# Optimization experiments

Hardware: AMD Instinct MI355X
Metric: run time of the kernel (lower is better)

Reference implementation:

```python
import jax, jax.numpy as jnp
import numpy as np

B, T, I, H = 128, 2048, 32, 64  # batch, seq_len, input_size, hidden_size
FF_SCALE = 0.001


def setup_inputs() -> dict:
    key = jax.random.key(0)
    ks = jax.random.split(key, 8)
    f32 = jnp.float32
    return {
        "x": jax.random.normal(ks[0], (B, T, I), f32),
        # forward-direction RNN params (torch layout: W_ih [H,I], W_hh [H,H])
        "W_ih_f": jax.random.normal(ks[1], (H, I), f32) * FF_SCALE,
        "W_hh_f": jnp.eye(H, dtype=f32),  # eye_ init * hidden_scale=1.0
        "b_ih_f": jnp.zeros((H,), f32),
        "b_hh_f": jnp.zeros((H,), f32),
        # backward-direction RNN params
        "W_ih_b": jax.random.normal(ks[2], (H, I), f32) * FF_SCALE,
        "W_hh_b": jnp.eye(H, dtype=f32),
        "b_ih_b": jnp.zeros((H,), f32),
        "b_hh_b": jnp.zeros((H,), f32),
        # MLP head: Linear(2H,2H) + leaky_relu + Linear(2H,1)
        "ff0_w": jax.random.normal(ks[3], (2 * H, 2 * H), f32) * FF_SCALE,
        "ff0_b": jnp.zeros((2 * H,), f32),
        "ff1_w": jax.random.normal(ks[4], (1, 2 * H), f32) * FF_SCALE,
        "ff1_b": jnp.zeros((1,), f32),
    }


def _rnn_dir(x, W_ih, W_hh, b_ih, b_hh, reverse):
    # Precompute input projection for all timesteps: [B,T,H]
    xw = jnp.einsum('bti,hi->bth', x, W_ih) + b_ih + b_hh

    def step(h, xt):
        h = jax.nn.relu(xt + h @ W_hh.T)
        return h, h

    h0 = jnp.zeros((x.shape[0], W_hh.shape[0]), x.dtype)
    # scan over time ([T,B,H]); reverse=True = reversed input + reversed output,
    # exactly the backward direction of a bidirectional RNN.
    _, hs = jax.lax.scan(step, h0, jnp.swapaxes(xw, 0, 1), reverse=reverse)
    return jnp.swapaxes(hs, 0, 1)  # [B,T,H]


def reference(x, W_ih_f, W_hh_f, b_ih_f, b_hh_f,
              W_ih_b, W_hh_b, b_ih_b, b_hh_b,
              ff0_w, ff0_b, ff1_w, ff1_b):
    hf = _rnn_dir(x, W_ih_f, W_hh_f, b_ih_f, b_hh_f, reverse=False)
    hb = _rnn_dir(x, W_ih_b, W_hh_b, b_ih_b, b_hh_b, reverse=True)
    h = jnp.concatenate([hf, hb], axis=-1)  # [B,T,2H]
    out = jax.nn.leaky_relu(h @ ff0_w.T + ff0_b, negative_slope=0.01)
    out = out @ ff1_w.T + ff1_b  # [B,T,1]
    return out
```

## Files before the change

kernel.cpp:

```cpp
#include <hip/hip_runtime.h>

#define BB 128
#define TT 2048
#define II 32
#define HH 64

typedef __attribute__((ext_vector_type(8))) short bf16x8;
typedef __attribute__((ext_vector_type(4))) float f32x4;

__device__ __forceinline__ unsigned f2bf(float f) {
    unsigned u = __builtin_bit_cast(unsigned, f);
    return (u + 0x7fffu + ((u >> 16) & 1u)) >> 16;
}

__device__ __forceinline__ unsigned cvtpk(float lo, float hi) {
    unsigned r;
    asm("v_cvt_pk_bf16_f32 %0, %1, %2" : "=v"(r) : "v"(lo), "v"(hi));
    return r;
}

__device__ __forceinline__ int swzW(int r, int t) {
    return (((r << 10) + t) ^ (((t >> 5) & 31) << 2)) ^ ((r & 7) << 2);
}

#define FWD_SEQ(M) \
  M(q0.x) M(q0.y) M(q0.z) M(q0.w) M(q1.x) M(q1.y) M(q1.z) M(q1.w) \
  M(q2.x) M(q2.y) M(q2.z) M(q2.w) M(q3.x) M(q3.y) M(q3.z) M(q3.w) \
  M(q4.x) M(q4.y) M(q4.z) M(q4.w) M(q5.x) M(q5.y) M(q5.z) M(q5.w) \
  M(q6.x) M(q6.y) M(q6.z) M(q6.w) M(q7.x) M(q7.y) M(q7.z) M(q7.w)
#define BWD_SEQ(M) \
  M(q7.w) M(q7.z) M(q7.y) M(q7.x) M(q6.w) M(q6.z) M(q6.y) M(q6.x) \
  M(q5.w) M(q5.z) M(q5.y) M(q5.x) M(q4.w) M(q4.z) M(q4.y) M(q4.x) \
  M(q3.w) M(q3.z) M(q3.y) M(q3.x) M(q2.w) M(q2.z) M(q2.y) M(q2.x) \
  M(q1.w) M(q1.z) M(q1.y) M(q1.x) M(q0.w) M(q0.z) M(q0.y) M(q0.x)

template<int DIR>
__device__ __noinline__ void rnn_serial_f(
    const float* __restrict__ Wih, const float* __restrict__ bih,
    const float* __restrict__ bhh, const float* __restrict__ Whh,
    const float* __restrict__ x, unsigned short* __restrict__ hbuf,
    int b, int lane, float (*hs)[HH])
{
    const float bias = bih[lane] + bhh[lane];
    const float4* wip = (const float4*)(Wih + lane * II);
    const float4* whp = (const float4*)(Whh + lane * HH);
    hs[0][lane] = 0.0f;
    unsigned short* hb = hbuf + ((size_t)(DIR * BB + b) * HH + lane) * TT;
    int cur = 0;
    for (int s = 0; s < TT; ++s) {
        const int t = DIR ? (TT - 1 - s) : s;
        const float4* xr = (const float4*)(x + ((size_t)b * TT + t) * II);
        float a0 = bias, a1 = 0.f, a2 = 0.f, a3 = 0.f;
        #pragma unroll
        for (int i4 = 0; i4 < II / 4; ++i4) {
            const float4 w4 = wip[i4];
            const float4 v  = xr[i4];
            a0 = fmaf(w4.x, v.x, a0); a1 = fmaf(w4.y, v.y, a1);
            a2 = fmaf(w4.z, v.z, a2); a3 = fmaf(w4.w, v.w, a3);
        }
        float s0 = 0.f, s1 = 0.f, s2 = 0.f, s3 = 0.f;
        const float* hc = hs[cur];
        #pragma unroll
        for (int j4 = 0; j4 < HH / 4; ++j4) {
            const float4 w4 = whp[j4];
            const float4 h4 = *(const float4*)(hc + 4 * j4);
            s0 = fmaf(w4.x, h4.x, s0); s1 = fmaf(w4.y, h4.y, s1);
            s2 = fmaf(w4.z, h4.z, s2); s3 = fmaf(w4.w, h4.w, s3);
        }
        const float h = fmaxf((a0 + a1) + (a2 + a3) + ((s0 + s1) + (s2 + s3)), 0.0f);
        hs[cur ^ 1][lane] = h;
        hb[t] = (unsigned short)f2bf(h);
        cur ^= 1;
    }
}

__global__ __launch_bounds__(512, 4) void rnn_fused_kernel(
    const float* __restrict__ x,
    const float* __restrict__ Wf, const float* __restrict__ bihf, const float* __restrict__ bhhf,
    const float* __restrict__ Wb, const float* __restrict__ bihb, const float* __restrict__ bhhb,
    const float* __restrict__ Whf, const float* __restrict__ Whb,
    unsigned short* __restrict__ hbuf)
{
    __shared__ __align__(16) float xwsh[8 * 1024];
    __shared__ __align__(16) unsigned short xst[2][8][512];
    __shared__ float sflags[2];
    __shared__ __align__(16) float hshd[2][2][HH];

    const int tid  = threadIdx.x;
    const int lane = tid & 63;
    const int wv   = __builtin_amdgcn_readfirstlane(tid >> 6);
    const int blk  = blockIdx.x;
    const int xcd  = blk & 7;
    const int rank = blk >> 3;
    const int b    = ((rank >> 4) << 3) | xcd;
    const int g    = rank & 15;
    const int g4   = g << 2;

    if (wv < 2) {
        const float* W = wv ? Whb : Whf;
        bool ok = true;
        const float4* wp = (const float4*)(W + lane * HH);
        #pragma unroll
        for (int j4 = 0; j4 < HH / 4; ++j4) {
            float4 v = wp[j4];
            ok &= (v.x == ((4*j4+0 == lane) ? 1.0f : 0.0f));
            ok &= (v.y == ((4*j4+1 == lane) ? 1.0f : 0.0f));
            ok &= (v.z == ((4*j4+2 == lane) ? 1.0f : 0.0f));
            ok &= (v.w == ((4*j4+3 == lane) ? 1.0f : 0.0f));
        }
        const bool isI = (__ballot(ok) == ~0ull);
        if (lane == 0) sflags[wv] = isI ? 1.0f : 0.0f;
    }
    __syncthreads();
    const bool iF = sflags[0] != 0.0f;
    const bool iB = sflags[1] != 0.0f;

    if (iF | iB) {
        bf16x8 afrag;
        {
            const int m = lane & 15, kg = lane >> 4;
            uint4 ap = {0u, 0u, 0u, 0u};
            if (m < 8) {
                const float* Wrow = ((m < 4) ? (Wf + (g4 + m) * II)
                                             : (Wb + (g4 + m - 4) * II)) + kg * 8;
                const float4 wa = *(const float4*)Wrow;
                const float4 wc = *(const float4*)(Wrow + 4);
                ap.x = cvtpk(wa.x, wa.y);
                ap.y = cvtpk(wa.z, wa.w);
                ap.z = cvtpk(wc.x, wc.y);
                ap.w = cvtpk(wc.z, wc.w);
            }
            afrag = __builtin_bit_cast(bf16x8, ap);
        }
        f32x4 cbias;
        {
            const int r0 = lane >> 4;
            #pragma unroll
            for (int j = 0; j < 4; ++j) {
                const int m = r0 * 4 + j;
                float v = 0.0f;
                if (m < 4)      v = bihf[g4 + m] + bhhf[g4 + m];
                else if (m < 8) v = bihb[g4 + m - 4] + bhhb[g4 + m - 4];
                cbias[j] = v;
            }
        }

        #define STAGE(BUFI, V0, V1) {                                           \
            unsigned short* bp_ = xst[BUFI][wv];                                \
            const int base_ = ((lane >> 3) << 5) + ((lane & 7) << 2);           \
            uint2 p_;                                                           \
            p_.x = cvtpk(V0.x, V0.y);                                           \
            p_.y = cvtpk(V0.z, V0.w);                                           \
            *(uint2*)(bp_ + base_) = p_;                                        \
            p_.x = cvtpk(V1.x, V1.y);                                           \
            p_.y = cvtpk(V1.z, V1.w);                                           \
            *(uint2*)(bp_ + base_ + 256) = p_;                                  \
        }

        float4 q0 = {0,0,0,0}, q1 = {0,0,0,0}, q2 = {0,0,0,0}, q3 = {0,0,0,0},
               q4 = {0,0,0,0}, q5 = {0,0,0,0}, q6 = {0,0,0,0}, q7 = {0,0,0,0};

        const float4* xb4 = (const float4*)(x + (size_t)b * TT * II) + (wv << 7);
        {
            const float4 a0 = xb4[lane], a1 = xb4[lane + 64];
            STAGE(0, a0, a1)
        }
        float4 va0 = xb4[1024 + lane], va1 = xb4[1024 + lane + 64];
        float4 vb0 = xb4[2048 + lane], vb1 = xb4[2048 + lane + 64];

        #pragma unroll
        for (int cc = 0; cc < 16; ++cc) {
            if (cc == 8) {
                __syncthreads();
                if ((lane >> 5) == 0) {
                    const int tb = (lane & 31) << 5;
                    q0 = *(const float4*)(xwsh + swzW(wv, tb + 0));
                    q1 = *(const float4*)(xwsh + swzW(wv, tb + 4));
                    q2 = *(const float4*)(xwsh + swzW(wv, tb + 8));
                    q3 = *(const float4*)(xwsh + swzW(wv, tb + 12));
                    q4 = *(const float4*)(xwsh + swzW(wv, tb + 16));
                    q5 = *(const float4*)(xwsh + swzW(wv, tb + 20));
                    q6 = *(const float4*)(xwsh + swzW(wv, tb + 24));
                    q7 = *(const float4*)(xwsh + swzW(wv, tb + 28));
                }
                __syncthreads();
            }
            const bf16x8 bfrag = *(const bf16x8*)(xst[cc & 1][wv] +
                ((lane & 15) << 5) + ((lane >> 4) << 3));
            float4 na0, na1;
            if (cc < 13) {
                const float4* gp = xb4 + ((cc + 3) << 10);
                na0 = gp[lane]; na1 = gp[lane + 64];
            }
            if (cc < 15) { STAGE((cc + 1) & 1, va0, va1) }
            {
                f32x4 accv = __builtin_amdgcn_mfma_f32_16x16x32_bf16(afrag, bfrag, cbias, 0, 0, 0);
                if (lane < 32) {
                    const int th = ((cc & 7) << 7) + (wv << 4) + (lane & 15);
                    const int m0 = (lane >> 4) << 2;
                    xwsh[swzW(m0 + 0, th)] = accv[0];
                    xwsh[swzW(m0 + 1, th)] = accv[1];
                    xwsh[swzW(m0 + 2, th)] = accv[2];
                    xwsh[swzW(m0 + 3, th)] = accv[3];
                }
            }
            va0 = vb0; va1 = vb1;
            vb0 = na0; vb1 = na1;
        }
        #undef STAGE

        __syncthreads();
        if ((lane >> 5) == 1) {
            const int tb = (lane & 31) << 5;
            q0 = *(const float4*)(xwsh + swzW(wv, tb + 0));
            q1 = *(const float4*)(xwsh + swzW(wv, tb + 4));
            q2 = *(const float4*)(xwsh + swzW(wv, tb + 8));
            q3 = *(const float4*)(xwsh + swzW(wv, tb + 12));
            q4 = *(const float4*)(xwsh + swzW(wv, tb + 16));
            q5 = *(const float4*)(xwsh + swzW(wv, tb + 20));
            q6 = *(const float4*)(xwsh + swzW(wv, tb + 24));
            q7 = *(const float4*)(xwsh + swzW(wv, tb + 28));
        }

        const int dir  = wv >> 2;
        const int hrow = g4 + (wv & 3);
        const bool en  = dir ? iB : iF;
        if (en) {
            float A = 0.0f, Bv = -__builtin_inff();
            #define CSTEP(c) { A = A + (c); Bv = fmaxf(Bv + (c), 0.0f); }
            if (dir == 0) { FWD_SEQ(CSTEP) } else { BWD_SEQ(CSTEP) }
            #undef CSTEP

            float h;
            if (dir == 0) {
                #pragma unroll
                for (int off = 1; off < 64; off <<= 1) {
                    float Au = __shfl_up(A,  (unsigned)off);
                    float Bu = __shfl_up(Bv, (unsigned)off);
                    if (lane >= off) {
                        Bv = fmaxf(Bu + A, Bv);
                        A  = Au + A;
                    }
                }
                float Ae = __shfl_up(A, 1u);
                float Be = __shfl_up(Bv, 1u);
                h = (lane == 0) ? 0.0f : fmaxf(Ae, Be);
            } else {
                #pragma unroll
                for (int off = 1; off < 64; off <<= 1) {
                    float Au = __shfl_down(A,  (unsigned)off);
                    float Bu = __shfl_down(Bv, (unsigned)off);
                    if (lane < 64 - off) {
                        Bv = fmaxf(Bu + A, Bv);
                        A  = Au + A;
                    }
                }
                float Ae = __shfl_down(A, 1u);
                float Be = __shfl_down(Bv, 1u);
                h = (lane == 63) ? 0.0f : fmaxf(Ae, Be);
            }

            #define ASTEP(c) { h = fmaxf(h + (c), 0.0f); (c) = h; }
            if (dir == 0) { FWD_SEQ(ASTEP) } else { BWD_SEQ(ASTEP) }
            #undef ASTEP

            unsigned short* hb = hbuf + ((size_t)(dir * BB + b) * HH + hrow) * TT + (lane << 5);
            uint4 s0q, s1q, s2q, s3q;
            s0q.x = cvtpk(q0.x, q0.y); s0q.y = cvtpk(q0.z, q0.w);
            s0q.z = cvtpk(q1.x, q1.y); s0q.w = cvtpk(q1.z, q1.w);
            s1q.x = cvtpk(q2.x, q2.y); s1q.y = cvtpk(q2.z, q2.w);
            s1q.z = cvtpk(q3.x, q3.y); s1q.w = cvtpk(q3.z, q3.w);
            s2q.x = cvtpk(q4.x, q4.y); s2q.y = cvtpk(q4.z, q4.w);
            s2q.z = cvtpk(q5.x, q5.y); s2q.w = cvtpk(q5.z, q5.w);
            s3q.x = cvtpk(q6.x, q6.y); s3q.y = cvtpk(q6.z, q6.w);
            s3q.z = cvtpk(q7.x, q7.y); s3q.w = cvtpk(q7.z, q7.w);
            uint4* hv = (uint4*)hb;
            hv[0] = s0q; hv[1] = s1q; hv[2] = s2q; hv[3] = s3q;
        }
    }

    if (!iF && g == 0 && wv == 0)
        rnn_serial_f<0>(Wf, bihf, bhhf, Whf, x, hbuf, b, lane, hshd[0]);
    if (!iB && g == 0 && wv == 1)
        rnn_serial_f<1>(Wb, bihb, bhhb, Whb, x, hbuf, b, lane, hshd[1]);
}

__global__ __launch_bounds__(256) void mlp_kernel(
    const unsigned short* __restrict__ hbuf,
    const float* __restrict__ w0, const float* __restrict__ b0,
    const float* __restrict__ w1, const float* __restrict__ b1,
    float* __restrict__ out)
{
    const int tid  = threadIdx.x;
    const int lane = tid & 63;
    const int wv   = tid >> 6;
    const int blk  = blockIdx.x;
    const int b    = blk >> 5;
    const int t0   = (blk & 31) << 6;

    __shared__ __align__(16) unsigned int w0dw[128 * 64];
    __shared__ __align__(16) unsigned int hsh[128 * 32];

    #pragma unroll
    for (int it = 0; it < 16; ++it) {
        const int q = it * 256 + tid;
        const float4 v = ((const float4*)w0)[q];
        uint2 p;
        p.x = cvtpk(v.x, v.y);
        p.y = cvtpk(v.z, v.w);
        const int k  = q >> 5;
        const int dw = (k << 6) + ((q & 31) << 1);
        *(uint2*)(w0dw + (dw ^ ((k & 15) << 2))) = p;
    }

    #pragma unroll
    for (int it = 0; it < 4; ++it) {
        const int q   = it * 256 + tid;
        const int j   = q >> 3, sub = q & 7;
        const unsigned short* rp =
            hbuf + ((size_t)((j >> 6) * BB + b) * HH + (j & 63)) * TT + t0;
        const uint4 v = *(const uint4*)(rp + sub * 8);
        const int dwb = j * 32 + sub * 4;
        *(uint4*)(hsh + (dwb ^ (((j >> 3) & 3) << 3))) = v;
    }
    __syncthreads();

    const int lg = lane >> 4;
    const int tl = (wv << 4) + (lane & 15);
    const int t  = t0 + tl;
    const int m  = lane & 15;

    f32x4 acc[8];
    #pragma unroll
    for (int kt = 0; kt < 8; ++kt) {
        const float4 v = *(const float4*)(b0 + kt * 16 + lg * 4);
        acc[kt][0] = v.x; acc[kt][1] = v.y; acc[kt][2] = v.z; acc[kt][3] = v.w;
    }

    const unsigned short* hus = (const unsigned short*)hsh;
    #pragma unroll
    for (int jt = 0; jt < 4; ++jt) {
        bf16x8 bf;
        #pragma unroll
        for (int i = 0; i < 8; ++i) {
            const int j  = jt * 32 + lg * 8 + i;
            const int dw = (j * 32 + (tl >> 1)) ^ (lg << 3);
            bf[i] = (short)hus[dw * 2 + (tl & 1)];
        }
        #pragma unroll
        for (int kt = 0; kt < 8; ++kt) {
            const int krow = kt * 16 + m;
            const bf16x8 af = *(const bf16x8*)(w0dw +
                ((((krow << 6) + (jt << 4) + (lg << 2)) ^ ((krow & 15) << 2))));
            acc[kt] = __builtin_amdgcn_mfma_f32_16x16x32_bf16(af, bf, acc[kt], 0, 0, 0);
        }
    }

    float o = 0.0f;
    #pragma unroll
    for (int kt = 0; kt < 8; ++kt) {
        const float4 wq = *(const float4*)(w1 + kt * 16 + lg * 4);
        float v0 = acc[kt][0]; v0 = fmaxf(v0, 0.01f * v0); o = fmaf(v0, wq.x, o);
        float v1 = acc[kt][1]; v1 = fmaxf(v1, 0.01f * v1); o = fmaf(v1, wq.y, o);
        float v2 = acc[kt][2]; v2 = fmaxf(v2, 0.01f * v2); o = fmaf(v2, wq.z, o);
        float v3 = acc[kt][3]; v3 = fmaxf(v3, 0.01f * v3); o = fmaf(v3, wq.w, o);
    }
    o += __shfl_xor(o, 16);
    o += __shfl_xor(o, 32);
    if (lg == 0) out[(size_t)b * TT + t] = o + b1[0];
}

extern "C" void kernel_launch(void* const* d_in, const int* in_sizes, int n_in,
                              void* d_out, int out_size, void* d_ws, size_t ws_size,
                              hipStream_t stream) {
    (void)in_sizes; (void)n_in; (void)out_size; (void)ws_size;
    const float* x    = (const float*)d_in[0];
    const float* Wihf = (const float*)d_in[1];
    const float* Whhf = (const float*)d_in[2];
    const float* bihf = (const float*)d_in[3];
    const float* bhhf = (const float*)d_in[4];
    const float* Wihb = (const float*)d_in[5];
    const float* Whhb = (const float*)d_in[6];
    const float* bihb = (const float*)d_in[7];
    const float* bhhb = (const float*)d_in[8];
    const float* ff0w = (const float*)d_in[9];
    const float* ff0b = (const float*)d_in[10];
    const float* ff1w = (const float*)d_in[11];
    const float* ff1b = (const float*)d_in[12];
    unsigned short* hbuf = (unsigned short*)d_ws;

    rnn_fused_kernel<<<dim3(16 * BB), dim3(512), 0, stream>>>(
        x, Wihf, bihf, bhhf, Wihb, bihb, bhhb, Whhf, Whhb, hbuf);
    mlp_kernel<<<dim3(BB * (TT / 64)), dim3(256), 0, stream>>>(
        hbuf, ff0w, ff0b, ff1w, ff1b, (float*)d_out);
}
```

Baseline: 168.9 us.

## Fill all MFMA rows with 8 hidden rows per direction and halve the grid

Each block now covers 8 forward and 8 backward hidden rows, so all 16 rows of the 16x16x32 MFMA carry real weights instead of 8, and the grid drops from 16×B to 8×B blocks. This halves the redundant global reads and bf16 staging of x that every block repeats. Each wave now runs both the forward and the backward closed-form scan for its hidden row. The projection buffer is snapshotted in four quarter passes with a new swizzle, which adds extra barriers and roughly doubles per-thread register state for the two q arrays, so occupancy may drop.

Result: slower. 176.1 us (+4.3%).

```diff
diff --git a/kernel.cpp b/kernel.cpp
--- a/kernel.cpp
+++ b/kernel.cpp
@@ -19,8 +19,8 @@
     return r;
 }
 
-__device__ __forceinline__ int swzW(int r, int t) {
-    return (((r << 10) + t) ^ (((t >> 5) & 31) << 2)) ^ ((r & 7) << 2);
+__device__ __forceinline__ int swzQ(int r, int t) {
+    return (((r << 9) + t) ^ (((t >> 5) & 15) << 2)) ^ (((r >> 2) & 1) << 4);
 }
 
 #define FWD_SEQ(M) \
@@ -81,7 +81,7 @@
     const float* __restrict__ Whf, const float* __restrict__ Whb,
     unsigned short* __restrict__ hbuf)
 {
-    __shared__ __align__(16) float xwsh[8 * 1024];
+    __shared__ __align__(16) float xwsh[16 * 512];
     __shared__ __align__(16) unsigned short xst[2][8][512];
     __shared__ float sflags[2];
     __shared__ __align__(16) float hshd[2][2][HH];
@@ -92,9 +92,8 @@
     const int blk  = blockIdx.x;
     const int xcd  = blk & 7;
     const int rank = blk >> 3;
-    const int b    = ((rank >> 4) << 3) | xcd;
-    const int g    = rank & 15;
-    const int g4   = g << 2;
+    const int b    = ((rank >> 3) << 3) | xcd;
+    const int g8   = (rank & 7) << 3;
 
     if (wv < 2) {
         const float* W = wv ? Whb : Whf;
@@ -119,17 +118,15 @@
         bf16x8 afrag;
         {
             const int m = lane & 15, kg = lane >> 4;
-            uint4 ap = {0u, 0u, 0u, 0u};
-            if (m < 8) {
-                const float* Wrow = ((m < 4) ? (Wf + (g4 + m) * II)
-                                             : (Wb + (g4 + m - 4) * II)) + kg * 8;
-                const float4 wa = *(const float4*)Wrow;
-                const float4 wc = *(const float4*)(Wrow + 4);
-                ap.x = cvtpk(wa.x, wa.y);
-                ap.y = cvtpk(wa.z, wa.w);
-                ap.z = cvtpk(wc.x, wc.y);
-                ap.w = cvtpk(wc.z, wc.w);
-            }
+            const float* Wrow = ((m < 8) ? (Wf + (g8 + m) * II)
+                                         : (Wb + (g8 + m - 8) * II)) + kg * 8;
+            const float4 wa = *(const float4*)Wrow;
+            const float4 wc = *(const float4*)(Wrow + 4);
+            uint4 ap;
+            ap.x = cvtpk(wa.x, wa.y);
+            ap.y = cvtpk(wa.z, wa.w);
+            ap.z = cvtpk(wc.x, wc.y);
+            ap.w = cvtpk(wc.z, wc.w);
             afrag = __builtin_bit_cast(bf16x8, ap);
         }
         f32x4 cbias;
@@ -137,11 +134,9 @@
             const int r0 = lane >> 4;
             #pragma unroll
             for (int j = 0; j < 4; ++j) {
-                const int m = r0 * 4 + j;
-                float v = 0.0f;
-                if (m < 4)      v = bihf[g4 + m] + bhhf[g4 + m];
-                else if (m < 8) v = bihb[g4 + m - 4] + bhhb[g4 + m - 4];
-                cbias[j] = v;
+                const int mc = r0 * 4 + j;
+                cbias[j] = (mc < 8) ? (bihf[g8 + mc] + bhhf[g8 + mc])
+                                    : (bihb[g8 + mc - 8] + bhhb[g8 + mc - 8]);
             }
         }
 
@@ -157,8 +152,32 @@
             *(uint2*)(bp_ + base_ + 256) = p_;                                  \
         }
 
-        float4 q0 = {0,0,0,0}, q1 = {0,0,0,0}, q2 = {0,0,0,0}, q3 = {0,0,0,0},
-               q4 = {0,0,0,0}, q5 = {0,0,0,0}, q6 = {0,0,0,0}, q7 = {0,0,0,0};
+        float4 qA0 = {0,0,0,0}, qA1 = {0,0,0,0}, qA2 = {0,0,0,0}, qA3 = {0,0,0,0},
+               qA4 = {0,0,0,0}, qA5 = {0,0,0,0}, qA6 = {0,0,0,0}, qA7 = {0,0,0,0};
+        float4 qB0 = {0,0,0,0}, qB1 = {0,0,0,0}, qB2 = {0,0,0,0}, qB3 = {0,0,0,0},
+               qB4 = {0,0,0,0}, qB5 = {0,0,0,0}, qB6 = {0,0,0,0}, qB7 = {0,0,0,0};
+
+        #define SNAPQ(QQ) {                                                     \
+            if ((lane >> 4) == (QQ)) {                                          \
+                const int tb = (lane & 15) << 5;                                \
+                qA0 = *(const float4*)(xwsh + swzQ(wv, tb + 0));                \
+                qA1 = *(const float4*)(xwsh + swzQ(wv, tb + 4));                \
+                qA2 = *(const float4*)(xwsh + swzQ(wv, tb + 8));                \
+                qA3 = *(const float4*)(xwsh + swzQ(wv, tb + 12));               \
+                qA4 = *(const float4*)(xwsh + swzQ(wv, tb + 16));               \
+                qA5 = *(const float4*)(xwsh + swzQ(wv, tb + 20));               \
+                qA6 = *(const float4*)(xwsh + swzQ(wv, tb + 24));               \
+                qA7 = *(const float4*)(xwsh + swzQ(wv, tb + 28));               \
+                qB0 = *(const float4*)(xwsh + swzQ(8 + wv, tb + 0));            \
+                qB1 = *(const float4*)(xwsh + swzQ(8 + wv, tb + 4));            \
+                qB2 = *(const float4*)(xwsh + swzQ(8 + wv, tb + 8));            \
+                qB3 = *(const float4*)(xwsh + swzQ(8 + wv, tb + 12));           \
+                qB4 = *(const float4*)(xwsh + swzQ(8 + wv, tb + 16));           \
+                qB5 = *(const float4*)(xwsh + swzQ(8 + wv, tb + 20));           \
+                qB6 = *(const float4*)(xwsh + swzQ(8 + wv, tb + 24));           \
+                qB7 = *(const float4*)(xwsh + swzQ(8 + wv, tb + 28));           \
+            }                                                                   \
+        }
 
         const float4* xb4 = (const float4*)(x + (size_t)b * TT * II) + (wv << 7);
         {
@@ -170,19 +189,9 @@
 
         #pragma unroll
         for (int cc = 0; cc < 16; ++cc) {
-            if (cc == 8) {
+            if (cc == 4 || cc == 8 || cc == 12) {
                 __syncthreads();
-                if ((lane >> 5) == 0) {
-                    const int tb = (lane & 31) << 5;
-                    q0 = *(const float4*)(xwsh + swzW(wv, tb + 0));
-                    q1 = *(const float4*)(xwsh + swzW(wv, tb + 4));
-                    q2 = *(const float4*)(xwsh + swzW(wv, tb + 8));
-                    q3 = *(const float4*)(xwsh + swzW(wv, tb + 12));
-                    q4 = *(const float4*)(xwsh + swzW(wv, tb + 16));
-                    q5 = *(const float4*)(xwsh + swzW(wv, tb + 20));
-                    q6 = *(const float4*)(xwsh + swzW(wv, tb + 24));
-                    q7 = *(const float4*)(xwsh + swzW(wv, tb + 28));
-                }
+                SNAPQ((cc >> 2) - 1)
                 __syncthreads();
             }
             const bf16x8 bfrag = *(const bf16x8*)(xst[cc & 1][wv] +
@@ -195,14 +204,12 @@
             if (cc < 15) { STAGE((cc + 1) & 1, va0, va1) }
             {
                 f32x4 accv = __builtin_amdgcn_mfma_f32_16x16x32_bf16(afrag, bfrag, cbias, 0, 0, 0);
-                if (lane < 32) {
-                    const int th = ((cc & 7) << 7) + (wv << 4) + (lane & 15);
-                    const int m0 = (lane >> 4) << 2;
-                    xwsh[swzW(m0 + 0, th)] = accv[0];
-                    xwsh[swzW(m0 + 1, th)] = accv[1];
-                    xwsh[swzW(m0 + 2, th)] = accv[2];
-                    xwsh[swzW(m0 + 3, th)] = accv[3];
-                }
+                const int th = ((cc & 3) << 7) + (wv << 4) + (lane & 15);
+                const int m0 = (lane >> 4) << 2;
+                xwsh[swzQ(m0 + 0, th)] = accv[0];
+                xwsh[swzQ(m0 + 1, th)] = accv[1];
+                xwsh[swzQ(m0 + 2, th)] = accv[2];
+                xwsh[swzQ(m0 + 3, th)] = accv[3];
             }
             va0 = vb0; va1 = vb1;
             vb0 = na0; vb1 = na1;
@@ -210,61 +217,34 @@
         #undef STAGE
 
         __syncthreads();
-        if ((lane >> 5) == 1) {
-            const int tb = (lane & 31) << 5;
-            q0 = *(const float4*)(xwsh + swzW(wv, tb + 0));
-            q1 = *(const float4*)(xwsh + swzW(wv, tb + 4));
-            q2 = *(const float4*)(xwsh + swzW(wv, tb + 8));
-            q3 = *(const float4*)(xwsh + swzW(wv, tb + 12));
-            q4 = *(const float4*)(xwsh + swzW(wv, tb + 16));
-            q5 = *(const float4*)(xwsh + swzW(wv, tb + 20));
-            q6 = *(const float4*)(xwsh + swzW(wv, tb + 24));
-            q7 = *(const float4*)(xwsh + swzW(wv, tb + 28));
-        }
-
-        const int dir  = wv >> 2;
-        const int hrow = g4 + (wv & 3);
-        const bool en  = dir ? iB : iF;
-        if (en) {
+        SNAPQ(3)
+        #undef SNAPQ
+
+        const int hrow = g8 + wv;
+
+        if (iF) {
+            float4 q0 = qA0, q1 = qA1, q2 = qA2, q3 = qA3,
+                   q4 = qA4, q5 = qA5, q6 = qA6, q7 = qA7;
             float A = 0.0f, Bv = -__builtin_inff();
             #define CSTEP(c) { A = A + (c); Bv = fmaxf(Bv + (c), 0.0f); }
-            if (dir == 0) { FWD_SEQ(CSTEP) } else { BWD_SEQ(CSTEP) }
+            FWD_SEQ(CSTEP)
             #undef CSTEP
-
-            float h;
-            if (dir == 0) {
-                #pragma unroll
-                for (int off = 1; off < 64; off <<= 1) {
-                    float Au = __shfl_up(A,  (unsigned)off);
-                    float Bu = __shfl_up(Bv, (unsigned)off);
-                    if (lane >= off) {
-                        Bv = fmaxf(Bu + A, Bv);
-                        A  = Au + A;
-                    }
+            #pragma unroll
+            for (int off = 1; off < 64; off <<= 1) {
+                float Au = __shfl_up(A,  (unsigned)off);
+                float Bu = __shfl_up(Bv, (unsigned)off);
+                if (lane >= off) {
+                    Bv = fmaxf(Bu + A, Bv);
+                    A  = Au + A;
                 }
-                float Ae = __shfl_up(A, 1u);
-                float Be = __shfl_up(Bv, 1u);
-                h = (lane == 0) ? 0.0f : fmaxf(Ae, Be);
-            } else {
-                #pragma unroll
-                for (int off = 1; off < 64; off <<= 1) {
-                    float Au = __shfl_down(A,  (unsigned)off);
-                    float Bu = __shfl_down(Bv, (unsigned)off);
-                    if (lane < 64 - off) {
-                        Bv = fmaxf(Bu + A, Bv);
-                        A  = Au + A;
-                    }
-                }
-                float Ae = __shfl_down(A, 1u);
-                float Be = __shfl_down(Bv, 1u);
-                h = (lane == 63) ? 0.0f : fmaxf(Ae, Be);
-            }
-
+            }
+            float Ae = __shfl_up(A, 1u);
+            float Be = __shfl_up(Bv, 1u);
+            float h = (lane == 0) ? 0.0f : fmaxf(Ae, Be);
             #define ASTEP(c) { h = fmaxf(h + (c), 0.0f); (c) = h; }
-            if (dir == 0) { FWD_SEQ(ASTEP) } else { BWD_SEQ(ASTEP) }
+            FWD_SEQ(ASTEP)
             #undef ASTEP
-
-            unsigned short* hb = hbuf + ((size_t)(dir * BB + b) * HH + hrow) * TT + (lane << 5);
+            unsigned short* hb = hbuf + ((size_t)b * HH + hrow) * TT + (lane << 5);
             uint4 s0q, s1q, s2q, s3q;
             s0q.x = cvtpk(q0.x, q0.y); s0q.y = cvtpk(q0.z, q0.w);
             s0q.z = cvtpk(q1.x, q1.y); s0q.w = cvtpk(q1.z, q1.w);
@@ -277,11 +257,47 @@
             uint4* hv = (uint4*)hb;
             hv[0] = s0q; hv[1] = s1q; hv[2] = s2q; hv[3] = s3q;
         }
-    }
-
-    if (!iF && g == 0 && wv == 0)
+
+        if (iB) {
+            float4 q0 = qB0, q1 = qB1, q2 = qB2, q3 = qB3,
+                   q4 = qB4, q5 = qB5, q6 = qB6, q7 = qB7;
+            float A = 0.0f, Bv = -__builtin_inff();
+            #define CSTEP(c) { A = A + (c); Bv = fmaxf(Bv + (c), 0.0f); }
+            BWD_SEQ(CSTEP)
+            #undef CSTEP
+            #pragma unroll
+            for (int off = 1; off < 64; off <<= 1) {
+                float Au = __shfl_down(A,  (unsigned)off);
+                float Bu = __shfl_down(Bv, (unsigned)off);
+                if (lane < 64 - off) {
+                    Bv = fmaxf(Bu + A, Bv);
+                    A  = Au + A;
+                }
+            }
+            float Ae = __shfl_down(A, 1u);
+            float Be = __shfl_down(Bv, 1u);
+            float h = (lane == 63) ? 0.0f : fmaxf(Ae, Be);
+            #define ASTEP(c) { h = fmaxf(h + (c), 0.0f); (c) = h; }
+            BWD_SEQ(ASTEP)
+            #undef ASTEP
+            unsigned short* hb = hbuf + ((size_t)(BB + b) * HH + hrow) * TT + (lane << 5);
+            uint4 s0q, s1q, s2q, s3q;
+            s0q.x = cvtpk(q0.x, q0.y); s0q.y = cvtpk(q0.z, q0.w);
+            s0q.z = cvtpk(q1.x, q1.y); s0q.w = cvtpk(q1.z, q1.w);
+            s1q.x = cvtpk(q2.x, q2.y); s1q.y = cvtpk(q2.z, q2.w);
+            s1q.z = cvtpk(q3.x, q3.y); s1q.w = cvtpk(q3.z, q3.w);
+            s2q.x = cvtpk(q4.x, q4.y); s2q.y = cvtpk(q4.z, q4.w);
+            s2q.z = cvtpk(q5.x, q5.y); s2q.w = cvtpk(q5.z, q5.w);
+            s3q.x = cvtpk(q6.x, q6.y); s3q.y = cvtpk(q6.z, q6.w);
+            s3q.z = cvtpk(q7.x, q7.y); s3q.w = cvtpk(q7.z, q7.w);
+            uint4* hv = (uint4*)hb;
+            hv[0] = s0q; hv[1] = s1q; hv[2] = s2q; hv[3] = s3q;
+        }
+    }
+
+    if (!iF && (rank & 7) == 0 && wv == 0)
         rnn_serial_f<0>(Wf, bihf, bhhf, Whf, x, hbuf, b, lane, hshd[0]);
-    if (!iB && g == 0 && wv == 1)
+    if (!iB && (rank & 7) == 0 && wv == 1)
         rnn_serial_f<1>(Wb, bihb, bhhb, Whb, x, hbuf, b, lane, hshd[1]);
 }
 
@@ -389,7 +405,7 @@
     const float* ff1b = (const float*)d_in[12];
     unsigned short* hbuf = (unsigned short*)d_ws;
 
-    rnn_fused_kernel<<<dim3(16 * BB), dim3(512), 0, stream>>>(
+    rnn_fused_kernel<<<dim3(8 * BB), dim3(512), 0, stream>>>(
         x, Wihf, bihf, bhhf, Wihb, bihb, bhhb, Whhf, Whhb, hbuf);
     mlp_kernel<<<dim3(BB * (TT / 64)), dim3(256), 0, stream>>>(
         hbuf, ff0w, ff0b, ff1w, ff1b, (float*)d_out);
```
